# Optimization experiments

Measured on AMD Instinct MI355X. Metric: run time of the kernel, lower is better.

## Reference

```python
import jax, jax.numpy as jnp
import numpy as np
from jax import lax

B, H0, W0 = 4, 64, 64
IN_DIM = 256; DIM = 256; HEADS = 8; WS = 8; HID = 1024
DH = DIM // HEADS          # 32, per-head dim
P = 16; K = 16             # DES decomposition: 256 = K * P


def hardswish(x):
    return x * jnp.clip(x + 3.0, 0.0, 6.0) * (1.0 / 6.0)


def layernorm(x, w, b):
    mu = jnp.mean(x, -1, keepdims=True)
    var = jnp.mean(jnp.square(x - mu), -1, keepdims=True)
    return (x - mu) * lax.rsqrt(var + 1e-5) * w + b


def dwconv(x, w, b, pad):
    # x: (B,C,H,W); w: (C,1,k,k) depthwise
    y = lax.conv_general_dilated(x, w, (1, 1), [(pad, pad), (pad, pad)],
                                 dimension_numbers=('NCHW', 'OIHW', 'NCHW'),
                                 feature_group_count=x.shape[1])
    return y + b[None, :, None, None]


def cross_attn(q, k, v, H, W, ws, d, scale, horizontal):
    # q,k,v: (B, N=H*W, C); C = h*d with h heads of dim d
    Bn, N, C = q.shape
    h = C // d
    if horizontal:
        G = H // ws
        def win(y):
            return y.reshape(Bn, G, ws, W, h, d).transpose(0, 1, 4, 2, 3, 5).reshape(Bn, G, h, ws * W, d)
    else:
        G = W // ws
        def win(y):
            return y.reshape(Bn, H, G, ws, h, d).transpose(0, 2, 4, 3, 1, 5).reshape(Bn, G, h, ws * H, d)
    qw, kw, vw = win(q), win(k), win(v)
    a = jax.nn.softmax(jnp.einsum('bghnd,bghmd->bghnm', qw, kw) * scale, axis=-1)
    o = jnp.einsum('bghnm,bghmd->bghnd', a, vw)
    if horizontal:
        o = o.reshape(Bn, G, h, ws, W, d).transpose(0, 1, 3, 4, 2, 5).reshape(Bn, H * W, C)
    else:
        o = o.reshape(Bn, G, h, ws, H, d).transpose(0, 4, 1, 3, 2, 5).reshape(Bn, H * W, C)
    return o


def setup_inputs() -> dict:
    key = jax.random.key(0)
    ks = jax.random.split(key, 12)
    r = lambda k, shape, s=0.02: jax.random.normal(k, shape, jnp.float32) * s
    return dict(
        x=jax.random.normal(ks[0], (B, H0 * W0, IN_DIM), jnp.float32),
        H=H0, W=W0,
        ln1_w=jnp.ones(IN_DIM, jnp.float32), ln1_b=jnp.zeros(IN_DIM, jnp.float32),
        Wqkv=r(ks[1], (IN_DIM, 2 * DIM)), bqkv=jnp.zeros(2 * DIM, jnp.float32),
        convp_w=r(ks[2], (DIM, 1, 3, 3), 0.1), convp_b=jnp.zeros(DIM, jnp.float32),
        Wout=r(ks[3], (DIM, DIM)), bout=jnp.zeros(DIM, jnp.float32),
        bn_g=jnp.ones(DIM, jnp.float32), bn_b=jnp.zeros(DIM, jnp.float32),
        des_wr=r(ks[4], (P, P), 0.1), des_br=jnp.zeros(P, jnp.float32),
        des_wl=r(ks[5], (K, K), 0.1), des_bl=jnp.zeros(K, jnp.float32),
        ln2_w=jnp.ones(IN_DIM, jnp.float32), ln2_b=jnp.zeros(IN_DIM, jnp.float32),
        fc1_w=r(ks[6], (IN_DIM, HID)), fc1_b=jnp.zeros(HID, jnp.float32),
        mix3_w=r(ks[7], (HID // 2, 1, 3, 3), 0.1), mix3_b=jnp.zeros(HID // 2, jnp.float32),
        mix5_w=r(ks[8], (HID // 2, 1, 5, 5), 0.1), mix5_b=jnp.zeros(HID // 2, jnp.float32),
        fc2_w=r(ks[9], (HID, DIM)), fc2_b=jnp.zeros(DIM, jnp.float32),
    )


def reference(x, H, W, ln1_w, ln1_b, Wqkv, bqkv, convp_w, convp_b, Wout, bout,
              bn_g, bn_b, des_wr, des_br, des_wl, des_bl, ln2_w, ln2_b,
              fc1_w, fc1_b, mix3_w, mix3_b, mix5_w, mix5_b, fc2_w, fc2_b):
    Bn, N, _ = x.shape
    res = x
    # ---- attention branch ----
    xn = layernorm(x, ln1_w, ln1_b)
    qv = xn @ Wqkv + bqkv                      # (B,N,2*DIM)
    q, v = jnp.split(qv, 2, axis=-1)
    # parallel depthwise conv on hardswish(v)
    v_img = hardswish(v.reshape(Bn, H, W, DIM).transpose(0, 3, 1, 2))
    v_conv = dwconv(v_img, convp_w, convp_b, 1).reshape(Bn, DIM, N).transpose(0, 2, 1)
    # cross-shaped window attention (k = v, per HRViT)
    qh, qvv = jnp.split(q, 2, axis=-1)
    vh, vv = jnp.split(v, 2, axis=-1)
    scale = DH ** -0.5
    ah = cross_attn(qh, vh, vh, H, W, WS, DH, scale, True)    # horizontal stripes
    av = cross_attn(qvv, vv, vv, H, W, WS, DH, scale, False)  # vertical stripes
    a = hardswish(jnp.concatenate([ah, av], axis=-1) + v_conv)
    a = a @ Wout + bout
    # BatchNorm1d over flattened (B*N, DIM), training-mode batch stats, eps=1e-5
    af = a.reshape(Bn * N, DIM)
    mu = jnp.mean(af, 0)
    var = jnp.mean(jnp.square(af - mu), 0)
    a = ((af - mu) * lax.rsqrt(var + 1e-5) * bn_g + bn_b).reshape(Bn, N, DIM)
    # DES shortcut on the residual
    xd = res.reshape(Bn, N, K, P) @ des_wr + des_br
    xd = jax.nn.gelu(xd.swapaxes(-1, -2), approximate=False)   # (B,N,P,K)
    xd = (xd @ des_wl + des_bl).swapaxes(-1, -2).reshape(Bn, N, DIM)
    x = a + xd + res
    # ---- MixCFN FFN branch ----
    res2 = x
    xn = layernorm(x, ln2_w, ln2_b)
    h1 = (xn @ fc1_w + fc1_b).transpose(0, 2, 1).reshape(Bn, HID, H, W)
    h1a, h1b = jnp.split(h1, 2, axis=1)
    hc = jnp.concatenate([dwconv(h1a, mix3_w, mix3_b, 1),
                          dwconv(h1b, mix5_w, mix5_b, 2)], axis=1)
    hc = jax.nn.gelu(hc, approximate=False).reshape(Bn, HID, N).transpose(0, 2, 1)
    return hc @ fc2_w + fc2_b + res2
```

## Files before the change

### kernel.cpp

```cpp
#include <hip/hip_runtime.h>
#include <hip/hip_bf16.h>

typedef __bf16 bf16;
typedef __bf16 bf16x8 __attribute__((ext_vector_type(8)));
typedef __bf16 bf16x4 __attribute__((ext_vector_type(4)));
typedef float f32x4 __attribute__((ext_vector_type(4)));

#define DEVFN static __device__ __forceinline__

DEVFN f32x4 mfma16(bf16x8 a, bf16x8 b, f32x4 c) {
  return __builtin_amdgcn_mfma_f32_16x16x32_bf16(a, b, c, 0, 0, 0);
}

DEVFN float hswish(float x) { return x * fminf(fmaxf(x + 3.f, 0.f), 6.f) * (1.f / 6.f); }
DEVFN float gelu_exact(float x) { return 0.5f * x * (1.f + erff(x * 0.70710678118654752f)); }

DEVFN unsigned packbf2(float lo, float hi) {
  union { bf16 h; unsigned short u; } a, b;
  a.h = (bf16)lo; b.h = (bf16)hi;
  return (unsigned)a.u | ((unsigned)b.u << 16);
}

DEVFN int tmap(int dir, int b, int g, int m) {
  return dir == 0 ? (b * 4096 + g * 512 + m)
                  : (b * 4096 + (m & 63) * 64 + g * 8 + (m >> 6));
}

__global__ __launch_bounds__(256) void convert_x(const float* __restrict__ src,
                                                 bf16* __restrict__ dst) {
  long i = ((long)blockIdx.x * 256 + threadIdx.x) * 8;
  f32x4 a = *(const f32x4*)(src + i);
  f32x4 b = *(const f32x4*)(src + i + 4);
  bf16x8 o;
#pragma unroll
  for (int j = 0; j < 4; j++) { o[j] = (bf16)a[j]; o[4 + j] = (bf16)b[j]; }
  *(bf16x8*)(dst + i) = o;
}

struct ConvArgs { const float* s[24]; bf16* d[24]; };

__global__ __launch_bounds__(256) void convert_w(ConvArgs a) {
  static const int cum[25] = {0, 131072, 196608, 458752, 720896, 723200, 727808, 740608,
                              740864, 741120, 741632, 741888, 742144, 742400, 742656,
                              742912, 742928, 743184, 743200, 743456, 743712, 744736,
                              745248, 745760, 746016};
  static const int Kt[7] = {256, 256, 256, 1024, 256, 512, 512};
  static const int Nt[7] = {512, 256, 1024, 256, 9, 9, 25};
  int g = blockIdx.x * 256 + threadIdx.x;
  if (g >= 746016) return;
  int e = 0;
  while (g >= cum[e + 1]) e++;
  int i = g - cum[e];
  float v = a.s[e][i];
  int di = i;
  if (e < 7) di = (i % Nt[e]) * Kt[e] + i / Nt[e];
  a.d[e][di] = (bf16)v;
}

__global__ __launch_bounds__(256) void ln_kernel(const bf16* __restrict__ x,
                                                 const bf16* __restrict__ w,
                                                 const bf16* __restrict__ b,
                                                 bf16* __restrict__ out) {
  int tid = threadIdx.x, lane = tid & 63, wv = tid >> 6;
  long row = (long)blockIdx.x * 4 + wv;
  bf16x4 xv = *(const bf16x4*)(x + row * 256 + lane * 4);
  float v[4];
#pragma unroll
  for (int i = 0; i < 4; i++) v[i] = (float)xv[i];
  float s = v[0] + v[1] + v[2] + v[3];
#pragma unroll
  for (int m = 1; m < 64; m <<= 1) s += __shfl_xor(s, m);
  float mu = s * (1.f / 256.f);
  float q = 0.f;
#pragma unroll
  for (int i = 0; i < 4; i++) { float d = v[i] - mu; q += d * d; }
#pragma unroll
  for (int m = 1; m < 64; m <<= 1) q += __shfl_xor(q, m);
  float r = rsqrtf(q * (1.f / 256.f) + 1e-5f);
  bf16x4 wv4 = *(const bf16x4*)(w + lane * 4);
  bf16x4 bv4 = *(const bf16x4*)(b + lane * 4);
  bf16x4 o;
#pragma unroll
  for (int i = 0; i < 4; i++) o[i] = (bf16)((v[i] - mu) * r * (float)wv4[i] + (float)bv4[i]);
  *(bf16x4*)(out + row * 256 + lane * 4) = o;
}

__global__ __launch_bounds__(256) void gemm_bt(const bf16* __restrict__ A,
                                               const bf16* __restrict__ BT,
                                               const bf16* __restrict__ bias,
                                               const bf16* __restrict__ resid,
                                               bf16* __restrict__ C,
                                               float* __restrict__ Cf,
                                               int M, int N, int K) {
  __shared__ __align__(16) bf16 Asl[128 * 32];
  __shared__ __align__(16) bf16 Bsl[128 * 32];
  const int tid = threadIdx.x;
  const int lane = tid & 63, wid = tid >> 6;
  const int rowBase = blockIdx.x * 128, colBase = blockIdx.y * 128;
  f32x4 acc[4][4] = {};
  const int e0 = wid * 1024 + lane * 8;
  const int e1 = e0 + 512;
  const int r0 = e0 >> 5, c0 = e0 & 31;
  const int r1 = e1 >> 5, c1 = e1 & 31;
  const bf16* Ab0 = A + (long)(rowBase + r0) * K + c0;
  const bf16* Ab1 = A + (long)(rowBase + r1) * K + c1;
  const bf16* Bb0 = BT + (long)(colBase + r0) * K + c0;
  const bf16* Bb1 = BT + (long)(colBase + r1) * K + c1;
  const int wr = (wid >> 1) * 64, wc = (wid & 1) * 64;
  const int fr = lane & 15, fk = (lane >> 4) * 8;
  for (int k0 = 0; k0 < K; k0 += 32) {
    bf16x8 a0 = *(const bf16x8*)(Ab0 + k0);
    bf16x8 a1 = *(const bf16x8*)(Ab1 + k0);
    bf16x8 b0 = *(const bf16x8*)(Bb0 + k0);
    bf16x8 b1 = *(const bf16x8*)(Bb1 + k0);
    __syncthreads();
    *(bf16x8*)&Asl[e0] = a0;
    *(bf16x8*)&Asl[e1] = a1;
    *(bf16x8*)&Bsl[e0] = b0;
    *(bf16x8*)&Bsl[e1] = b1;
    __syncthreads();
    bf16x8 af[4], bfv[4];
#pragma unroll
    for (int m = 0; m < 4; m++) af[m] = *(const bf16x8*)&Asl[(wr + m * 16 + fr) * 32 + fk];
#pragma unroll
    for (int n = 0; n < 4; n++) bfv[n] = *(const bf16x8*)&Bsl[(wc + n * 16 + fr) * 32 + fk];
#pragma unroll
    for (int m = 0; m < 4; m++)
#pragma unroll
      for (int n = 0; n < 4; n++) acc[m][n] = mfma16(af[m], bfv[n], acc[m][n]);
  }
#pragma unroll
  for (int m = 0; m < 4; m++) {
#pragma unroll
    for (int r = 0; r < 4; r++) {
      int row = rowBase + wr + m * 16 + (lane >> 4) * 4 + r;
#pragma unroll
      for (int n = 0; n < 4; n++) {
        int col = colBase + wc + n * 16 + fr;
        float v = acc[m][n][r] + (float)bias[col];
        if (resid) v += (float)resid[(long)row * N + col];
        if (Cf) Cf[(long)row * N + col] = v;
        else C[(long)row * N + col] = (bf16)v;
      }
    }
  }
}

__global__ __launch_bounds__(256) void dwconv_v(const bf16* __restrict__ qv,
                                                const bf16* __restrict__ wt,
                                                const bf16* __restrict__ cb,
                                                bf16* __restrict__ vconv) {
  int tid = threadIdx.x;
  int c0 = (tid & 31) * 8;
  int s = blockIdx.x * 8 + (tid >> 5);
  int h = (s >> 6) & 63, w2 = s & 63;
  long base = (long)(s >> 12) * 4096;
  float acc[8];
#pragma unroll
  for (int j = 0; j < 8; j++) acc[j] = (float)cb[c0 + j];
#pragma unroll
  for (int ky = -1; ky <= 1; ky++) {
    int hy = h + ky;
    if ((unsigned)hy >= 64u) continue;
#pragma unroll
    for (int kx = -1; kx <= 1; kx++) {
      int wx = w2 + kx;
      if ((unsigned)wx >= 64u) continue;
      long t = base + hy * 64 + wx;
      bf16x8 iv = *(const bf16x8*)(qv + t * 512 + 256 + c0);
      bf16x8 wvv = *(const bf16x8*)(wt + ((ky + 1) * 3 + (kx + 1)) * 256 + c0);
#pragma unroll
      for (int j = 0; j < 8; j++) acc[j] += hswish((float)iv[j]) * (float)wvv[j];
    }
  }
  bf16x8 o;
#pragma unroll
  for (int j = 0; j < 8; j++) o[j] = (bf16)acc[j];
  *(bf16x8*)(vconv + (long)s * 256 + c0) = o;
}

__global__ __launch_bounds__(256) void attn_kernel(const bf16* __restrict__ qv,
                                                   const bf16* __restrict__ vconv,
                                                   bf16* __restrict__ aout) {
  __shared__ __align__(16) bf16 Kl[512 * 32];
  __shared__ __align__(16) bf16 Vt[32 * 512];
  __shared__ __align__(16) bf16 Pl[4][16 * 40];
  const int tid = threadIdx.x, lane = tid & 63, wid = tid >> 6;
  const int u = blockIdx.x >> 1, hf = blockIdx.x & 1;
  const int head = u & 3, g = (u >> 2) & 7, dir = (u >> 5) & 1, b = u >> 6;
  const int qch = dir * 128 + head * 32;
  const int vch = 256 + qch;
  char* KlB = (char*)Kl;
  char* VtB = (char*)Vt;

#pragma unroll
  for (int it = 0; it < 8; it++) {
    int task = it * 256 + tid;
    int t = task >> 2, cg = task & 3;
    long tk = tmap(dir, b, g, t);
    bf16x8 v = *(const bf16x8*)(qv + tk * 512 + vch + cg * 8);
    int byte = (t * 64 + cg * 16) ^ ((t & 7) << 4);
    *(bf16x8*)(KlB + byte) = v;
  }
  __syncthreads();
#pragma unroll
  for (int it = 0; it < 8; it++) {
    int task = it * 256 + tid;
    int ch = task & 31, kvb = task >> 5;
    bf16 tv[8];
#pragma unroll
    for (int j = 0; j < 8; j++) {
      int kv = kvb * 8 + j;
      int byte = (kv * 64 + ch * 2) ^ ((kv & 7) << 4);
      tv[j] = *(const bf16*)(KlB + byte);
    }
    int wbyte = (ch * 1024 + kvb * 16) ^ ((ch & 7) << 4);
    *(bf16x8*)(VtB + wbyte) = *(bf16x8*)tv;
  }
  __syncthreads();

  const int fr = lane & 15, fkh = lane >> 4;
  const float scale = 0.17677669529663687f;
  const f32x4 zero = {0.f, 0.f, 0.f, 0.f};
  char* PlB = (char*)&Pl[wid][0];

  for (int qt = 0; qt < 4; ++qt) {
    int qrow0 = hf * 256 + wid * 64 + qt * 16;
    long tq = tmap(dir, b, g, qrow0 + fr);
    bf16x8 qf = *(const bf16x8*)(qv + tq * 512 + qch + fkh * 8);
    float m = 4.0f, l = 0.f;
    f32x4 o0 = zero, o1 = zero;
    const int wb0 = fr * 80 + fkh * 8;
    const int rb = fr * 80 + fkh * 16;
#pragma unroll
    for (int c = 0; c < 16; c++) {
      int kb0 = ((c * 32 + fr) * 64 + fkh * 16) ^ ((fr & 7) << 4);
      int kb1 = ((c * 32 + 16 + fr) * 64 + fkh * 16) ^ ((fr & 7) << 4);
      bf16x8 kf0 = *(const bf16x8*)(KlB + kb0);
      bf16x8 kf1 = *(const bf16x8*)(KlB + kb1);
      f32x4 s0 = mfma16(kf0, qf, zero);
      f32x4 s1 = mfma16(kf1, qf, zero);
      float cmax = -1e30f;
#pragma unroll
      for (int r = 0; r < 4; r++) {
        s0[r] *= scale; s1[r] *= scale;
        cmax = fmaxf(cmax, fmaxf(s0[r], s1[r]));
      }
      if (__any(cmax > m + 8.f)) {
        float cm = cmax;
        cm = fmaxf(cm, __shfl_xor(cm, 16));
        cm = fmaxf(cm, __shfl_xor(cm, 32));
        float mn = fmaxf(m, cm);
        float corr = __expf(m - mn);
        l *= corr;
        float c0c = __shfl(corr, fkh * 4 + 0);
        float c1c = __shfl(corr, fkh * 4 + 1);
        float c2c = __shfl(corr, fkh * 4 + 2);
        float c3c = __shfl(corr, fkh * 4 + 3);
        o0[0] *= c0c; o0[1] *= c1c; o0[2] *= c2c; o0[3] *= c3c;
        o1[0] *= c0c; o1[1] *= c1c; o1[2] *= c2c; o1[3] *= c3c;
        m = mn;
      }
      float p0[4], p1[4];
#pragma unroll
      for (int r = 0; r < 4; r++) {
        p0[r] = __expf(s0[r] - m);
        p1[r] = __expf(s1[r] - m);
        l += p0[r] + p1[r];
      }
      *(unsigned*)(PlB + wb0) = packbf2(p0[0], p0[1]);
      *(unsigned*)(PlB + wb0 + 4) = packbf2(p0[2], p0[3]);
      *(unsigned*)(PlB + wb0 + 32) = packbf2(p1[0], p1[1]);
      *(unsigned*)(PlB + wb0 + 36) = packbf2(p1[2], p1[3]);
      bf16x8 pa = *(const bf16x8*)(PlB + rb);
      int vb = ((c * 32 + fkh * 8) * 2) ^ ((fr & 7) << 4);
      bf16x8 v0 = *(const bf16x8*)(VtB + fr * 1024 + vb);
      bf16x8 v1 = *(const bf16x8*)(VtB + (16 + fr) * 1024 + vb);
      o0 = mfma16(pa, v0, o0);
      o1 = mfma16(pa, v1, o1);
    }
    float lt = l;
    lt += __shfl_xor(lt, 16);
    lt += __shfl_xor(lt, 32);
    float inv = 1.f / lt;
    float i0 = __shfl(inv, fkh * 4 + 0);
    float i1 = __shfl(inv, fkh * 4 + 1);
    float i2 = __shfl(inv, fkh * 4 + 2);
    float i3 = __shfl(inv, fkh * 4 + 3);
    float iv4[4] = {i0, i1, i2, i3};
#pragma unroll
    for (int r = 0; r < 4; r++) {
      int row = qrow0 + fkh * 4 + r;
      long to = tmap(dir, b, g, row);
      float vc0 = (float)vconv[to * 256 + qch + fr];
      float vc1 = (float)vconv[to * 256 + qch + 16 + fr];
      aout[to * 256 + qch + fr] = (bf16)hswish(o0[r] * iv4[r] + vc0);
      aout[to * 256 + qch + 16 + fr] = (bf16)hswish(o1[r] * iv4[r] + vc1);
    }
  }
}

__global__ __launch_bounds__(256) void bn_part(const bf16* __restrict__ a2,
                                               float* __restrict__ part) {
  int tid = threadIdx.x, bx = blockIdx.x;
  int c0 = (tid & 31) * 8, rg = tid >> 5;
  float s[8] = {}, q[8] = {};
  for (int i = 0; i < 32; i++) {
    long row = (long)bx * 256 + rg * 32 + i;
    bf16x8 v = *(const bf16x8*)(a2 + row * 256 + c0);
#pragma unroll
    for (int j = 0; j < 8; j++) { float f = (float)v[j]; s[j] += f; q[j] += f * f; }
  }
  long pb = (long)bx * 8 + rg;
#pragma unroll
  for (int j = 0; j < 8; j++) {
    part[pb * 256 + c0 + j] = s[j];
    part[131072 + pb * 256 + c0 + j] = q[j];
  }
}

__global__ void bn_final(const float* __restrict__ part, const bf16* __restrict__ g,
                         const bf16* __restrict__ bb, float* __restrict__ coef) {
  int c = threadIdx.x;
  float s = 0.f, q = 0.f;
  for (int i = 0; i < 512; i++) { s += part[i * 256 + c]; q += part[131072 + i * 256 + c]; }
  float mu = s * (1.f / 16384.f);
  float var = q * (1.f / 16384.f) - mu * mu;
  float sc = (float)g[c] * rsqrtf(var + 1e-5f);
  coef[c] = sc;
  coef[256 + c] = (float)bb[c] - mu * sc;
}

__global__ __launch_bounds__(256) void des_combine(const bf16* __restrict__ x,
                                                   const bf16* __restrict__ a2,
                                                   const float* __restrict__ coef,
                                                   const bf16* __restrict__ wr,
                                                   const bf16* __restrict__ br,
                                                   const bf16* __restrict__ wl,
                                                   const bf16* __restrict__ bl,
                                                   bf16* __restrict__ x2) {
  __shared__ float X[4][256], M1[4][256];
  __shared__ float WR[256], WL[256], BR[16], BL[16], SC[256], SH[256];
  int tid = threadIdx.x, lane = tid & 63, wvi = tid >> 6;
  WR[tid] = (float)wr[tid];
  WL[tid] = (float)wl[tid];
  SC[tid] = coef[tid];
  SH[tid] = coef[256 + tid];
  if (tid < 16) { BR[tid] = (float)br[tid]; BL[tid] = (float)bl[tid]; }
  long t = (long)blockIdx.x * 4 + wvi;
  bf16x4 xv = *(const bf16x4*)(x + t * 256 + lane * 4);
#pragma unroll
  for (int i = 0; i < 4; i++) X[wvi][lane * 4 + i] = (float)xv[i];
  __syncthreads();
#pragma unroll
  for (int u2 = 0; u2 < 4; u2++) {
    int e = u2 * 64 + lane, k = e >> 4, p = e & 15;
    float acc = BR[p];
#pragma unroll
    for (int p2 = 0; p2 < 16; p2++) acc += X[wvi][k * 16 + p2] * WR[p2 * 16 + p];
    M1[wvi][e] = gelu_exact(acc);
  }
  __syncthreads();
#pragma unroll
  for (int u2 = 0; u2 < 4; u2++) {
    int e = u2 * 64 + lane, k = e >> 4, p = e & 15;
    float acc = BL[k];
#pragma unroll
    for (int k2 = 0; k2 < 16; k2++) acc += M1[wvi][k2 * 16 + p] * WL[k2 * 16 + k];
    float a2v = (float)a2[t * 256 + e];
    x2[t * 256 + e] = (bf16)(SC[e] * a2v + SH[e] + acc + X[wvi][e]);
  }
}

__global__ __launch_bounds__(256) void mixconv(const bf16* __restrict__ h1,
                                               const bf16* __restrict__ wt3,
                                               const bf16* __restrict__ b3,
                                               const bf16* __restrict__ wt5,
                                               const bf16* __restrict__ b5,
                                               bf16* __restrict__ hc) {
  int bx = blockIdx.x;
  int slice = bx & 3, wh = (bx >> 2) & 1, h = (bx >> 3) & 63, b = bx >> 9;
  int tid = threadIdx.x;
  int c0 = slice * 256 + (tid & 31) * 8;
  int w0 = wh * 32 + (tid >> 5) * 4;
  bool five = slice >= 2;
  int cc = five ? c0 - 512 : c0;
  long base = (long)b * 4096;
  float acc[4][8];
  {
    const bf16* bp = (five ? b5 : b3) + cc;
#pragma unroll
    for (int q = 0; q < 8; q++) {
      float bv = (float)bp[q];
#pragma unroll
      for (int i = 0; i < 4; i++) acc[i][q] = bv;
    }
  }
  if (!five) {
    const bf16* wbase = wt3 + cc;
#pragma unroll
    for (int ky = 0; ky < 3; ky++) {
      int hy = h + ky - 1;
      if ((unsigned)hy >= 64u) continue;
      float row[6][8];
#pragma unroll
      for (int j = 0; j < 6; j++) {
        int wx = w0 + j - 1;
        bool valid = (unsigned)wx < 64u;
        int wxc = valid ? wx : 0;
        bf16x8 iv = *(const bf16x8*)(h1 + (base + hy * 64 + wxc) * 1024 + c0);
#pragma unroll
        for (int q = 0; q < 8; q++) row[j][q] = valid ? (float)iv[q] : 0.f;
      }
#pragma unroll
      for (int kx = 0; kx < 3; kx++) {
        bf16x8 wv = *(const bf16x8*)(wbase + (ky * 3 + kx) * 512);
        float wf[8];
#pragma unroll
        for (int q = 0; q < 8; q++) wf[q] = (float)wv[q];
#pragma unroll
        for (int i = 0; i < 4; i++)
#pragma unroll
          for (int q = 0; q < 8; q++) acc[i][q] += row[i + kx][q] * wf[q];
      }
    }
  } else {
    const bf16* wbase = wt5 + cc;
#pragma unroll
    for (int ky = 0; ky < 5; ky++) {
      int hy = h + ky - 2;
      if ((unsigned)hy >= 64u) continue;
      float row[8][8];
#pragma unroll
      for (int j = 0; j < 8; j++) {
        int wx = w0 + j - 2;
        bool valid = (unsigned)wx < 64u;
        int wxc = valid ? wx : 0;
        bf16x8 iv = *(const bf16x8*)(h1 + (base + hy * 64 + wxc) * 1024 + c0);
#pragma unroll
        for (int q = 0; q < 8; q++) row[j][q] = valid ? (float)iv[q] : 0.f;
      }
#pragma unroll
      for (int kx = 0; kx < 5; kx++) {
        bf16x8 wv = *(const bf16x8*)(wbase + (ky * 5 + kx) * 512);
        float wf[8];
#pragma unroll
        for (int q = 0; q < 8; q++) wf[q] = (float)wv[q];
#pragma unroll
        for (int i = 0; i < 4; i++)
#pragma unroll
          for (int q = 0; q < 8; q++) acc[i][q] += row[i + kx][q] * wf[q];
      }
    }
  }
#pragma unroll
  for (int i = 0; i < 4; i++) {
    long t = base + h * 64 + w0 + i;
    bf16x8 o;
#pragma unroll
    for (int q = 0; q < 8; q++) o[q] = (bf16)gelu_exact(acc[i][q]);
    *(bf16x8*)(hc + t * 1024 + c0) = o;
  }
}

extern "C" void kernel_launch(void* const* d_in, const int* in_sizes, int n_in,
                              void* d_out, int out_size, void* d_ws, size_t ws_size,
                              hipStream_t stream) {
  if (ws_size < 92274688ull) return;

  char* ws = (char*)d_ws;
  float* bncoef = (float*)(ws + 256);
  char* Dc = ws + 4096;
  auto alloc = [&](size_t bytes) { bf16* p = (bf16*)Dc; Dc += (bytes + 255) & ~(size_t)255; return p; };
  bf16* cx      = alloc(8388608);
  bf16* cWqkvT  = alloc(262144);
  bf16* cWoutT  = alloc(131072);
  bf16* cfc1T   = alloc(524288);
  bf16* cfc2T   = alloc(524288);
  bf16* cconvp  = alloc(4608);
  bf16* cwt3    = alloc(9216);
  bf16* cwt5    = alloc(25600);
  bf16* cln1w   = alloc(512);
  bf16* cln1b   = alloc(512);
  bf16* cbqkv   = alloc(1024);
  bf16* cconvpb = alloc(512);
  bf16* cbout   = alloc(512);
  bf16* cbng    = alloc(512);
  bf16* cbnb    = alloc(512);
  bf16* cdwr    = alloc(512);
  bf16* cdbr    = alloc(32);
  bf16* cdwl    = alloc(512);
  bf16* cdbl    = alloc(32);
  bf16* cln2w   = alloc(512);
  bf16* cln2b   = alloc(512);
  bf16* cfc1b   = alloc(2048);
  bf16* cm3b    = alloc(1024);
  bf16* cm5b    = alloc(1024);
  bf16* cfc2b   = alloc(512);
  bf16* qv    = (bf16*)(ws + 16777216);
  bf16* vconv = (bf16*)(ws + 33554432);
  bf16* attn  = (bf16*)(ws + 41943040);
  bf16* h1    = (bf16*)(ws + 16777216);
  bf16* xnb     = (bf16*)(ws + 50331648);
  bf16* a2      = (bf16*)(ws + 58720256);
  float* bnpart = (float*)(ws + 67108864);
  bf16* hc      = (bf16*)(ws + 50331648);
  bf16* x2 = (bf16*)(ws + 83886080);

  convert_x<<<2048, 256, 0, stream>>>((const float*)d_in[0], cx);
  ConvArgs ca;
  const int srcIdx[24] = {5, 9, 19, 25, 7, 21, 23, 3, 4, 6, 8, 10, 11, 12,
                          13, 14, 15, 16, 17, 18, 20, 22, 24, 26};
  bf16* dsts[24] = {cWqkvT, cWoutT, cfc1T, cfc2T, cconvp, cwt3, cwt5, cln1w, cln1b,
                    cbqkv, cconvpb, cbout, cbng, cbnb, cdwr, cdbr, cdwl, cdbl,
                    cln2w, cln2b, cfc1b, cm3b, cm5b, cfc2b};
  for (int i = 0; i < 24; i++) { ca.s[i] = (const float*)d_in[srcIdx[i]]; ca.d[i] = dsts[i]; }
  convert_w<<<2916, 256, 0, stream>>>(ca);

  ln_kernel<<<4096, 256, 0, stream>>>(cx, cln1w, cln1b, xnb);
  gemm_bt<<<dim3(128, 4), 256, 0, stream>>>(xnb, cWqkvT, cbqkv, nullptr, qv, nullptr, 16384, 512, 256);
  dwconv_v<<<2048, 256, 0, stream>>>(qv, cconvp, cconvpb, vconv);
  attn_kernel<<<512, 256, 0, stream>>>(qv, vconv, attn);
  gemm_bt<<<dim3(128, 2), 256, 0, stream>>>(attn, cWoutT, cbout, nullptr, a2, nullptr, 16384, 256, 256);
  bn_part<<<64, 256, 0, stream>>>(a2, bnpart);
  bn_final<<<1, 256, 0, stream>>>(bnpart, cbng, cbnb, bncoef);
  des_combine<<<4096, 256, 0, stream>>>(cx, a2, bncoef, cdwr, cdbr, cdwl, cdbl, x2);
  ln_kernel<<<4096, 256, 0, stream>>>(x2, cln2w, cln2b, xnb);
  gemm_bt<<<dim3(128, 8), 256, 0, stream>>>(xnb, cfc1T, cfc1b, nullptr, h1, nullptr, 16384, 1024, 256);
  mixconv<<<2048, 256, 0, stream>>>(h1, cwt3, cm3b, cwt5, cm5b, hc);
  gemm_bt<<<dim3(128, 2), 256, 0, stream>>>(hc, cfc2T, cfc2b, x2, nullptr, (float*)d_out, 16384, 256, 1024);
}
```

Baseline: 256.4 us.

## Keep softmax probabilities in registers and process two query tiles per pass

The attention kernel stops round-tripping the P matrix through per-wave shared memory. Instead it permutes the V-transpose layout so the MFMA accumulator output can be packed directly as the A operand. It also processes two 16-row query tiles per iteration, so each K and V fragment loaded from LDS is reused for both. This cuts LDS traffic and wait points, at the cost of higher register pressure and a more intricate key ordering in Vt.

After: 253.5 us. Within noise of the previous version (-1.2%).

```diff
diff --git a/kernel.cpp b/kernel.cpp
--- a/kernel.cpp
+++ b/kernel.cpp
@@ -184,7 +184,6 @@
                                                    bf16* __restrict__ aout) {
   __shared__ __align__(16) bf16 Kl[512 * 32];
   __shared__ __align__(16) bf16 Vt[32 * 512];
-  __shared__ __align__(16) bf16 Pl[4][16 * 40];
   const int tid = threadIdx.x, lane = tid & 63, wid = tid >> 6;
   const int u = blockIdx.x >> 1, hf = blockIdx.x & 1;
   const int head = u & 3, g = (u >> 2) & 7, dir = (u >> 5) & 1, b = u >> 6;
@@ -207,10 +206,11 @@
   for (int it = 0; it < 8; it++) {
     int task = it * 256 + tid;
     int ch = task & 31, kvb = task >> 5;
+    int c = kvb >> 2, fb = kvb & 3;
     bf16 tv[8];
 #pragma unroll
     for (int j = 0; j < 8; j++) {
-      int kv = kvb * 8 + j;
+      int kv = c * 32 + (j < 4 ? fb * 4 + j : 16 + fb * 4 + (j - 4));
       int byte = (kv * 64 + ch * 2) ^ ((kv & 7) << 4);
       tv[j] = *(const bf16*)(KlB + byte);
     }
@@ -222,80 +222,119 @@
   const int fr = lane & 15, fkh = lane >> 4;
   const float scale = 0.17677669529663687f;
   const f32x4 zero = {0.f, 0.f, 0.f, 0.f};
-  char* PlB = (char*)&Pl[wid][0];
-
-  for (int qt = 0; qt < 4; ++qt) {
-    int qrow0 = hf * 256 + wid * 64 + qt * 16;
-    long tq = tmap(dir, b, g, qrow0 + fr);
-    bf16x8 qf = *(const bf16x8*)(qv + tq * 512 + qch + fkh * 8);
-    float m = 4.0f, l = 0.f;
-    f32x4 o0 = zero, o1 = zero;
-    const int wb0 = fr * 80 + fkh * 8;
-    const int rb = fr * 80 + fkh * 16;
+
+  for (int qp = 0; qp < 2; ++qp) {
+    int qrowA = hf * 256 + wid * 64 + qp * 32;
+    int qrowB = qrowA + 16;
+    long tqA = tmap(dir, b, g, qrowA + fr);
+    long tqB = tmap(dir, b, g, qrowB + fr);
+    bf16x8 qfA = *(const bf16x8*)(qv + tqA * 512 + qch + fkh * 8);
+    bf16x8 qfB = *(const bf16x8*)(qv + tqB * 512 + qch + fkh * 8);
+    float mA = 4.0f, lA = 0.f, mB = 4.0f, lB = 0.f;
+    f32x4 oA0 = zero, oA1 = zero, oB0 = zero, oB1 = zero;
 #pragma unroll
     for (int c = 0; c < 16; c++) {
       int kb0 = ((c * 32 + fr) * 64 + fkh * 16) ^ ((fr & 7) << 4);
       int kb1 = ((c * 32 + 16 + fr) * 64 + fkh * 16) ^ ((fr & 7) << 4);
       bf16x8 kf0 = *(const bf16x8*)(KlB + kb0);
       bf16x8 kf1 = *(const bf16x8*)(KlB + kb1);
-      f32x4 s0 = mfma16(kf0, qf, zero);
-      f32x4 s1 = mfma16(kf1, qf, zero);
-      float cmax = -1e30f;
+      int vb = ((c * 32 + fkh * 8) * 2) ^ ((fr & 7) << 4);
+      bf16x8 v0 = *(const bf16x8*)(VtB + fr * 1024 + vb);
+      bf16x8 v1 = *(const bf16x8*)(VtB + (16 + fr) * 1024 + vb);
+      f32x4 sA0 = mfma16(kf0, qfA, zero);
+      f32x4 sA1 = mfma16(kf1, qfA, zero);
+      f32x4 sB0 = mfma16(kf0, qfB, zero);
+      f32x4 sB1 = mfma16(kf1, qfB, zero);
+      float cmaxA = -1e30f, cmaxB = -1e30f;
 #pragma unroll
       for (int r = 0; r < 4; r++) {
-        s0[r] *= scale; s1[r] *= scale;
-        cmax = fmaxf(cmax, fmaxf(s0[r], s1[r]));
-      }
-      if (__any(cmax > m + 8.f)) {
-        float cm = cmax;
+        sA0[r] *= scale; sA1[r] *= scale;
+        sB0[r] *= scale; sB1[r] *= scale;
+        cmaxA = fmaxf(cmaxA, fmaxf(sA0[r], sA1[r]));
+        cmaxB = fmaxf(cmaxB, fmaxf(sB0[r], sB1[r]));
+      }
+      if (__any(cmaxA > mA + 8.f)) {
+        float cm = cmaxA;
         cm = fmaxf(cm, __shfl_xor(cm, 16));
         cm = fmaxf(cm, __shfl_xor(cm, 32));
-        float mn = fmaxf(m, cm);
-        float corr = __expf(m - mn);
-        l *= corr;
+        float mn = fmaxf(mA, cm);
+        float corr = __expf(mA - mn);
+        lA *= corr;
         float c0c = __shfl(corr, fkh * 4 + 0);
         float c1c = __shfl(corr, fkh * 4 + 1);
         float c2c = __shfl(corr, fkh * 4 + 2);
         float c3c = __shfl(corr, fkh * 4 + 3);
-        o0[0] *= c0c; o0[1] *= c1c; o0[2] *= c2c; o0[3] *= c3c;
-        o1[0] *= c0c; o1[1] *= c1c; o1[2] *= c2c; o1[3] *= c3c;
-        m = mn;
-      }
-      float p0[4], p1[4];
+        oA0[0] *= c0c; oA0[1] *= c1c; oA0[2] *= c2c; oA0[3] *= c3c;
+        oA1[0] *= c0c; oA1[1] *= c1c; oA1[2] *= c2c; oA1[3] *= c3c;
+        mA = mn;
+      }
+      if (__any(cmaxB > mB + 8.f)) {
+        float cm = cmaxB;
+        cm = fmaxf(cm, __shfl_xor(cm, 16));
+        cm = fmaxf(cm, __shfl_xor(cm, 32));
+        float mn = fmaxf(mB, cm);
+        float corr = __expf(mB - mn);
+        lB *= corr;
+        float c0c = __shfl(corr, fkh * 4 + 0);
+        float c1c = __shfl(corr, fkh * 4 + 1);
+        float c2c = __shfl(corr, fkh * 4 + 2);
+        float c3c = __shfl(corr, fkh * 4 + 3);
+        oB0[0] *= c0c; oB0[1] *= c1c; oB0[2] *= c2c; oB0[3] *= c3c;
+        oB1[0] *= c0c; oB1[1] *= c1c; oB1[2] *= c2c; oB1[3] *= c3c;
+        mB = mn;
+      }
+      float pA0[4], pA1[4], pB0[4], pB1[4];
 #pragma unroll
       for (int r = 0; r < 4; r++) {
-        p0[r] = __expf(s0[r] - m);
-        p1[r] = __expf(s1[r] - m);
-        l += p0[r] + p1[r];
-      }
-      *(unsigned*)(PlB + wb0) = packbf2(p0[0], p0[1]);
-      *(unsigned*)(PlB + wb0 + 4) = packbf2(p0[2], p0[3]);
-      *(unsigned*)(PlB + wb0 + 32) = packbf2(p1[0], p1[1]);
-      *(unsigned*)(PlB + wb0 + 36) = packbf2(p1[2], p1[3]);
-      bf16x8 pa = *(const bf16x8*)(PlB + rb);
-      int vb = ((c * 32 + fkh * 8) * 2) ^ ((fr & 7) << 4);
-      bf16x8 v0 = *(const bf16x8*)(VtB + fr * 1024 + vb);
-      bf16x8 v1 = *(const bf16x8*)(VtB + (16 + fr) * 1024 + vb);
-      o0 = mfma16(pa, v0, o0);
-      o1 = mfma16(pa, v1, o1);
-    }
-    float lt = l;
-    lt += __shfl_xor(lt, 16);
-    lt += __shfl_xor(lt, 32);
-    float inv = 1.f / lt;
-    float i0 = __shfl(inv, fkh * 4 + 0);
-    float i1 = __shfl(inv, fkh * 4 + 1);
-    float i2 = __shfl(inv, fkh * 4 + 2);
-    float i3 = __shfl(inv, fkh * 4 + 3);
-    float iv4[4] = {i0, i1, i2, i3};
+        pA0[r] = __expf(sA0[r] - mA);
+        pA1[r] = __expf(sA1[r] - mA);
+        pB0[r] = __expf(sB0[r] - mB);
+        pB1[r] = __expf(sB1[r] - mB);
+        lA += pA0[r] + pA1[r];
+        lB += pB0[r] + pB1[r];
+      }
+      union { unsigned u[4]; bf16x8 v8; } paA, paB;
+      paA.u[0] = packbf2(pA0[0], pA0[1]);
+      paA.u[1] = packbf2(pA0[2], pA0[3]);
+      paA.u[2] = packbf2(pA1[0], pA1[1]);
+      paA.u[3] = packbf2(pA1[2], pA1[3]);
+      paB.u[0] = packbf2(pB0[0], pB0[1]);
+      paB.u[1] = packbf2(pB0[2], pB0[3]);
+      paB.u[2] = packbf2(pB1[0], pB1[1]);
+      paB.u[3] = packbf2(pB1[2], pB1[3]);
+      oA0 = mfma16(paA.v8, v0, oA0);
+      oA1 = mfma16(paA.v8, v1, oA1);
+      oB0 = mfma16(paB.v8, v0, oB0);
+      oB1 = mfma16(paB.v8, v1, oB1);
+    }
+    float ltA = lA;
+    ltA += __shfl_xor(ltA, 16);
+    ltA += __shfl_xor(ltA, 32);
+    float invA = 1.f / ltA;
+    float ltB = lB;
+    ltB += __shfl_xor(ltB, 16);
+    ltB += __shfl_xor(ltB, 32);
+    float invB = 1.f / ltB;
+    float iA[4], iB[4];
 #pragma unroll
     for (int r = 0; r < 4; r++) {
-      int row = qrow0 + fkh * 4 + r;
-      long to = tmap(dir, b, g, row);
-      float vc0 = (float)vconv[to * 256 + qch + fr];
-      float vc1 = (float)vconv[to * 256 + qch + 16 + fr];
-      aout[to * 256 + qch + fr] = (bf16)hswish(o0[r] * iv4[r] + vc0);
-      aout[to * 256 + qch + 16 + fr] = (bf16)hswish(o1[r] * iv4[r] + vc1);
+      iA[r] = __shfl(invA, fkh * 4 + r);
+      iB[r] = __shfl(invB, fkh * 4 + r);
+    }
+#pragma unroll
+    for (int r = 0; r < 4; r++) {
+      int rowA = qrowA + fkh * 4 + r;
+      long toA = tmap(dir, b, g, rowA);
+      float vc0 = (float)vconv[toA * 256 + qch + fr];
+      float vc1 = (float)vconv[toA * 256 + qch + 16 + fr];
+      aout[toA * 256 + qch + fr] = (bf16)hswish(oA0[r] * iA[r] + vc0);
+      aout[toA * 256 + qch + 16 + fr] = (bf16)hswish(oA1[r] * iA[r] + vc1);
+      int rowB = qrowB + fkh * 4 + r;
+      long toB = tmap(dir, b, g, rowB);
+      float wc0 = (float)vconv[toB * 256 + qch + fr];
+      float wc1 = (float)vconv[toB * 256 + qch + 16 + fr];
+      aout[toB * 256 + qch + fr] = (bf16)hswish(oB0[r] * iB[r] + wc0);
+      aout[toB * 256 + qch + 16 + fr] = (bf16)hswish(oB1[r] * iB[r] + wc1);
     }
   }
 }
```
